# Optimization experiments

Hardware: AMD Instinct MI355X
Metric: run time of the kernel (lower is better)

The kernel has to match this reference:

```python
import jax, jax.numpy as jnp
import numpy as np

NV = 16384
NF = 32768
B = 4


def _build_laplacian(nv, nf, seed=0):
    # Faithful replication of the torch module's __init__ laplacian construction.
    rng = np.random.RandomState(seed)
    faces = rng.randint(0, nv, size=(nf, 3)).astype(np.int64)
    lap = np.zeros((nv, nv), dtype=np.float32)
    lap[faces[:, 0], faces[:, 1]] = -1
    lap[faces[:, 1], faces[:, 0]] = -1
    lap[faces[:, 1], faces[:, 2]] = -1
    lap[faces[:, 2], faces[:, 1]] = -1
    lap[faces[:, 2], faces[:, 0]] = -1
    lap[faces[:, 0], faces[:, 2]] = -1
    r, c = np.diag_indices(nv)
    lap[r, c] = -lap.sum(1)
    deg = lap[r, c]  # degree per vertex (>= 0)
    # vectorized version of: for i: if lap[i,i] > 0: lap[i,:] /= lap[i,i]
    scale = np.where(deg > 0, 1.0 / np.maximum(deg, 1.0), 1.0).astype(np.float32)
    lap = lap * scale[:, None]
    return lap


def setup_inputs() -> dict:
    key = jax.random.key(0)
    x = jax.random.normal(key, (B, NV, 3), dtype=jnp.float32)
    laplacian = jnp.asarray(_build_laplacian(NV, NF))
    return {"x": x, "laplacian": laplacian}


def reference(x, laplacian):
    # y[b, i, d] = sum_j L[i, j] * x[b, j, d]
    y = jnp.einsum("ij,bjd->bid", laplacian, x)
    # squared L2 norm per batch element (sum over all non-batch dims)
    loss = jnp.sum(y * y, axis=(1, 2))  # [B]
    return loss
```

## Files before the change

### kernel.cpp

```cpp
#include <hip/hip_runtime.h>

#define NV 16384
#define BROWS 32
#define JT 256
#define NT (NV / JT)
#define THREADS 256

typedef const __attribute__((address_space(1))) void* as1_ptr;
typedef __attribute__((address_space(3))) void* as3_ptr;

__device__ __forceinline__ void gload_lds16(const float* g, float* l) {
  __builtin_amdgcn_global_load_lds((as1_ptr)g, (as3_ptr)l, 16, 0, 0);
}

#define FENCE asm volatile("" ::: "memory")
#define WAITV(n) asm volatile("s_waitcnt vmcnt(" #n ")" ::: "memory")

__global__ __launch_bounds__(THREADS, 2) void lap_loss_kernel(
    const float* __restrict__ x, const float* __restrict__ L,
    float* __restrict__ out) {
  __shared__ float lbuf[2][BROWS][JT];

  const int lane = threadIdx.x & 63;
  const int w    = threadIdx.x >> 6;
  const size_t i0 = (size_t)blockIdx.x * BROWS;

  const float* gL[8];
#pragma unroll
  for (int r = 0; r < 8; ++r)
    gL[r] = L + (i0 + 8 * w + r) * NV + lane * 4;

  const float* gx = x + (size_t)w * NV * 3 + lane * 12;

  float acc[BROWS][3];
#pragma unroll
  for (int r = 0; r < BROWS; ++r)
#pragma unroll
    for (int d = 0; d < 3; ++d) acc[r][d] = 0.f;

  float4 xc0 = *(const float4*)(gx + 0);
  float4 xc1 = *(const float4*)(gx + 4);
  float4 xc2 = *(const float4*)(gx + 8);
  FENCE;
#pragma unroll
  for (int r = 0; r < 8; ++r)
    gload_lds16(gL[r], &lbuf[0][8 * w + r][0]);

#pragma unroll 1
  for (int t = 0; t < NT; ++t) {
    const int cur = t & 1;

    float4 xn0, xn1, xn2;
    if (t + 1 < NT) {
      const float* gxn = gx + (size_t)(t + 1) * JT * 3;
      xn0 = *(const float4*)(gxn + 0);
      xn1 = *(const float4*)(gxn + 4);
      xn2 = *(const float4*)(gxn + 8);
    }
    FENCE;

    if (t + 1 < NT) {
#pragma unroll
      for (int r = 0; r < 8; ++r)
        gload_lds16(gL[r] + (size_t)(t + 1) * JT, &lbuf[cur ^ 1][8 * w + r][0]);
      WAITV(8);
    } else {
      WAITV(0);
    }
    __builtin_amdgcn_s_barrier();
    FENCE;

    {
      const float xf[12] = {xc0.x, xc0.y, xc0.z, xc0.w,
                            xc1.x, xc1.y, xc1.z, xc1.w,
                            xc2.x, xc2.y, xc2.z, xc2.w};
#pragma unroll
      for (int r = 0; r < BROWS; ++r) {
        float4 lv = *(const float4*)&lbuf[cur][r][lane * 4];
        const float lf[4] = {lv.x, lv.y, lv.z, lv.w};
#pragma unroll
        for (int jj = 0; jj < 4; ++jj)
#pragma unroll
          for (int d = 0; d < 3; ++d)
            acc[r][d] = fmaf(lf[jj], xf[jj * 3 + d], acc[r][d]);
      }
    }

    FENCE;
    __builtin_amdgcn_s_barrier();
    FENCE;

    xc0 = xn0; xc1 = xn1; xc2 = xn2;
  }

  float s = 0.f;
#pragma unroll
  for (int r = 0; r < BROWS; ++r)
#pragma unroll
    for (int d = 0; d < 3; ++d) {
      float v = acc[r][d];
#pragma unroll
      for (int off = 32; off > 0; off >>= 1)
        v += __shfl_xor(v, off, 64);
      s += v * v;
    }

  if (lane == 0) atomicAdd(&out[w], s);
}

extern "C" void kernel_launch(void* const* d_in, const int* in_sizes, int n_in,
                              void* d_out, int out_size, void* d_ws, size_t ws_size,
                              hipStream_t stream) {
  const float* x = (const float*)d_in[0];
  const float* L = (const float*)d_in[1];
  float* out = (float*)d_out;

  hipMemsetAsync(out, 0, out_size * sizeof(float), stream);

  const int nblocks = NV / BROWS;
  lap_loss_kernel<<<nblocks, THREADS, 0, stream>>>(x, L, out);
}
```

Measured before the change: 230.6 us.

## Use single-wave blocks computing all batches to remove workgroup barriers

Each workgroup becomes a single 64-lane wave that handles 8 Laplacian rows for all 4 batch elements, instead of four waves (one per batch) sharing 32 rows. Because one wave owns its LDS slice, the s_barrier pairs go away. Synchronisation now uses only vmcnt waits, and the last tile is peeled out of the loop. The trade-off is that x is re-read by four times as many blocks, and each wave holds a larger register footprint (48 x values plus 96 accumulators), which may limit occupancy.

```diff
diff --git a/kernel.cpp b/kernel.cpp
--- a/kernel.cpp
+++ b/kernel.cpp
@@ -1,10 +1,9 @@
 #include <hip/hip_runtime.h>
 
 #define NV 16384
-#define BROWS 32
 #define JT 256
 #define NT (NV / JT)
-#define THREADS 256
+#define ROWS 8
 
 typedef const __attribute__((address_space(1))) void* as1_ptr;
 typedef __attribute__((address_space(3))) void* as3_ptr;
@@ -16,96 +15,112 @@
 #define FENCE asm volatile("" ::: "memory")
 #define WAITV(n) asm volatile("s_waitcnt vmcnt(" #n ")" ::: "memory")
 
-__global__ __launch_bounds__(THREADS, 2) void lap_loss_kernel(
+__global__ __launch_bounds__(64, 2) void lap_loss_kernel(
     const float* __restrict__ x, const float* __restrict__ L,
     float* __restrict__ out) {
-  __shared__ float lbuf[2][BROWS][JT];
+  __shared__ float lbuf[2][ROWS][JT];
 
   const int lane = threadIdx.x & 63;
-  const int w    = threadIdx.x >> 6;
-  const size_t i0 = (size_t)blockIdx.x * BROWS;
+  const size_t i0 = (size_t)blockIdx.x * ROWS;
 
-  const float* gL[8];
+  const float* gL[ROWS];
 #pragma unroll
-  for (int r = 0; r < 8; ++r)
-    gL[r] = L + (i0 + 8 * w + r) * NV + lane * 4;
+  for (int r = 0; r < ROWS; ++r) gL[r] = L + (i0 + r) * NV + lane * 4;
 
-  const float* gx = x + (size_t)w * NV * 3 + lane * 12;
+  const float* gx[4];
+#pragma unroll
+  for (int b = 0; b < 4; ++b) gx[b] = x + (size_t)b * NV * 3 + lane * 12;
 
-  float acc[BROWS][3];
+  float acc[ROWS][4][3];
 #pragma unroll
-  for (int r = 0; r < BROWS; ++r)
+  for (int r = 0; r < ROWS; ++r)
 #pragma unroll
-    for (int d = 0; d < 3; ++d) acc[r][d] = 0.f;
+    for (int b = 0; b < 4; ++b)
+#pragma unroll
+      for (int d = 0; d < 3; ++d) acc[r][b][d] = 0.f;
 
-  float4 xc0 = *(const float4*)(gx + 0);
-  float4 xc1 = *(const float4*)(gx + 4);
-  float4 xc2 = *(const float4*)(gx + 8);
+  float4 xn[12];
+  float  xf[48];
+
+#pragma unroll
+  for (int b = 0; b < 4; ++b) {
+    const float4* p = (const float4*)gx[b];
+    xn[b * 3 + 0] = p[0]; xn[b * 3 + 1] = p[1]; xn[b * 3 + 2] = p[2];
+  }
   FENCE;
 #pragma unroll
-  for (int r = 0; r < 8; ++r)
-    gload_lds16(gL[r], &lbuf[0][8 * w + r][0]);
+  for (int r = 0; r < ROWS; ++r) gload_lds16(gL[r], &lbuf[0][r][0]);
+  FENCE;
+#pragma unroll
+  for (int i = 0; i < 12; ++i) {
+    xf[i * 4 + 0] = xn[i].x; xf[i * 4 + 1] = xn[i].y;
+    xf[i * 4 + 2] = xn[i].z; xf[i * 4 + 3] = xn[i].w;
+  }
+
+  auto body = [&](int t, int cur) {
+#pragma unroll
+    for (int r = 0; r < ROWS; ++r) {
+      float4 lv = *(const float4*)&lbuf[cur][r][lane * 4];
+      const float lf[4] = {lv.x, lv.y, lv.z, lv.w};
+#pragma unroll
+      for (int q = 0; q < 4; ++q)
+#pragma unroll
+        for (int b = 0; b < 4; ++b)
+#pragma unroll
+          for (int d = 0; d < 3; ++d)
+            acc[r][b][d] =
+                fmaf(lf[q], xf[b * 12 + q * 3 + d], acc[r][b][d]);
+    }
+  };
 
 #pragma unroll 1
-  for (int t = 0; t < NT; ++t) {
+  for (int t = 0; t < NT - 1; ++t) {
     const int cur = t & 1;
 
-    float4 xn0, xn1, xn2;
-    if (t + 1 < NT) {
-      const float* gxn = gx + (size_t)(t + 1) * JT * 3;
-      xn0 = *(const float4*)(gxn + 0);
-      xn1 = *(const float4*)(gxn + 4);
-      xn2 = *(const float4*)(gxn + 8);
+#pragma unroll
+    for (int b = 0; b < 4; ++b) {
+      const float4* p = (const float4*)(gx[b] + (size_t)(t + 1) * JT * 3);
+      xn[b * 3 + 0] = p[0]; xn[b * 3 + 1] = p[1]; xn[b * 3 + 2] = p[2];
     }
     FENCE;
+#pragma unroll
+    for (int r = 0; r < ROWS; ++r)
+      gload_lds16(gL[r] + (size_t)(t + 1) * JT, &lbuf[cur ^ 1][r][0]);
+    FENCE;
+    WAITV(20);
 
-    if (t + 1 < NT) {
+    body(t, cur);
+
+    __builtin_amdgcn_sched_barrier(0);
+    WAITV(8);
 #pragma unroll
-      for (int r = 0; r < 8; ++r)
-        gload_lds16(gL[r] + (size_t)(t + 1) * JT, &lbuf[cur ^ 1][8 * w + r][0]);
-      WAITV(8);
-    } else {
-      WAITV(0);
+    for (int i = 0; i < 12; ++i) {
+      xf[i * 4 + 0] = xn[i].x; xf[i * 4 + 1] = xn[i].y;
+      xf[i * 4 + 2] = xn[i].z; xf[i * 4 + 3] = xn[i].w;
     }
-    __builtin_amdgcn_s_barrier();
-    FENCE;
-
-    {
-      const float xf[12] = {xc0.x, xc0.y, xc0.z, xc0.w,
-                            xc1.x, xc1.y, xc1.z, xc1.w,
-                            xc2.x, xc2.y, xc2.z, xc2.w};
-#pragma unroll
-      for (int r = 0; r < BROWS; ++r) {
-        float4 lv = *(const float4*)&lbuf[cur][r][lane * 4];
-        const float lf[4] = {lv.x, lv.y, lv.z, lv.w};
-#pragma unroll
-        for (int jj = 0; jj < 4; ++jj)
-#pragma unroll
-          for (int d = 0; d < 3; ++d)
-            acc[r][d] = fmaf(lf[jj], xf[jj * 3 + d], acc[r][d]);
-      }
-    }
-
-    FENCE;
-    __builtin_amdgcn_s_barrier();
-    FENCE;
-
-    xc0 = xn0; xc1 = xn1; xc2 = xn2;
   }
 
-  float s = 0.f;
+  WAITV(0);
+  body(NT - 1, (NT - 1) & 1);
+
+  float s[4] = {0.f, 0.f, 0.f, 0.f};
 #pragma unroll
-  for (int r = 0; r < BROWS; ++r)
+  for (int r = 0; r < ROWS; ++r)
 #pragma unroll
-    for (int d = 0; d < 3; ++d) {
-      float v = acc[r][d];
+    for (int b = 0; b < 4; ++b)
 #pragma unroll
-      for (int off = 32; off > 0; off >>= 1)
-        v += __shfl_xor(v, off, 64);
-      s += v * v;
-    }
+      for (int d = 0; d < 3; ++d) {
+        float v = acc[r][b][d];
+#pragma unroll
+        for (int off = 32; off > 0; off >>= 1)
+          v += __shfl_xor(v, off, 64);
+        s[b] += v * v;
+      }
 
-  if (lane == 0) atomicAdd(&out[w], s);
+  if (lane == 0) {
+#pragma unroll
+    for (int b = 0; b < 4; ++b) atomicAdd(&out[b], s[b]);
+  }
 }
 
 extern "C" void kernel_launch(void* const* d_in, const int* in_sizes, int n_in,
@@ -117,6 +132,6 @@
 
   hipMemsetAsync(out, 0, out_size * sizeof(float), stream);
 
-  const int nblocks = NV / BROWS;
-  lap_loss_kernel<<<nblocks, THREADS, 0, stream>>>(x, L, out);
+  const int nblocks = NV / ROWS;
+  lap_loss_kernel<<<nblocks, 64, 0, stream>>>(x, L, out);
 }
```

After: 290.1 us. 1.26x slower.
